# Optimization experiments

Measured on AMD Instinct MI355X. Metric: run time of the kernel, lower is better.

## Reference

```python
import jax, jax.numpy as jnp
import numpy as np

B, N, D = 4, 2048, 1024
H, DH = 16, 64
MAX_POS_EMB = 256
TOPK = 64


def setup_inputs() -> dict:
    key = jax.random.key(0)
    ks = jax.random.split(key, 8)
    s = 0.02
    inner = H * DH
    return {
        "x": jax.random.normal(ks[0], (B, N, D), jnp.float32),
        "gating_mask": jax.random.uniform(ks[1], (B, 1, N, 1), jnp.float32),
        "Wq": jax.random.normal(ks[2], (D, inner), jnp.float32) * s,
        "bq": jnp.zeros((inner,), jnp.float32),
        "Wkv": jax.random.normal(ks[3], (D, 2 * inner), jnp.float32) * s,
        "bkv": jnp.zeros((2 * inner,), jnp.float32),
        "Wo": jax.random.normal(ks[4], (inner, D), jnp.float32) * s,
        "bo": jnp.zeros((D,), jnp.float32),
        "rel_emb": jax.random.normal(ks[5], (MAX_POS_EMB, DH), jnp.float32) * s,
        "mask": jnp.ones((B, N), bool),
        "sparse_topk": TOPK,
    }


def reference(x, gating_mask, Wq, bq, Wkv, bkv, Wo, bo, rel_emb, mask, sparse_topk):
    b, n, d = x.shape
    h, dh = H, DH
    scale = dh ** -0.5
    mask_val = -jnp.finfo(x.dtype).max

    # projections -> [b, h, n, dh]
    q = (x @ Wq + bq).reshape(b, n, h, dh).transpose(0, 2, 1, 3)
    kv = x @ Wkv + bkv
    k = kv[..., : h * dh].reshape(b, n, h, dh).transpose(0, 2, 1, 3)
    v = kv[..., h * dh:].reshape(b, n, h, dh).transpose(0, 2, 1, 3)

    dots = jnp.einsum("bhid,bhjd->bhij", q, k) * scale  # [b,h,n,n]

    # relative positional bias: q . E[clip(i-j+M, 0, M-1)]
    seq = jnp.arange(n)
    dist = jnp.clip(seq[:, None] - seq[None, :] + MAX_POS_EMB, 0, MAX_POS_EMB - 1)
    qE = jnp.einsum("bhid,rd->bhir", q, rel_emb) * scale  # [b,h,n,R]
    pos_attn = jnp.take_along_axis(qE, dist[None, None, :, :], axis=-1)  # [b,h,n,n]
    dots = dots + pos_attn

    # padding mask: mask_i * mask_j
    full_mask = mask[:, None, :, None] & mask[:, None, None, :]
    dots = jnp.where(full_mask, dots, mask_val)

    # topk sparsification: keep only scores >= k-th largest per row
    top = jax.lax.top_k(dots, sparse_topk)[0]  # [b,h,n,topk]
    vk = top[..., -1:]
    dots = jnp.where(dots < vk, mask_val, dots)

    attn = jax.nn.softmax(dots, axis=-1)
    attn = attn * gating_mask

    out = jnp.einsum("bhij,bhjd->bhid", attn, v)
    out = out.transpose(0, 2, 1, 3).reshape(b, n, h * dh)
    return out @ Wo + bo
```

## Files before the change

kernel.cpp:

```cpp
#include <hip/hip_runtime.h>
#include <stdint.h>


typedef __attribute__((ext_vector_type(8))) short short8;
typedef __attribute__((ext_vector_type(4))) float floatx4;

#define Bn   4
#define Nn   2048
#define Hn   16
#define BHn  (Bn*Hn)
#define DELTA 0.00125f

__device__ __forceinline__ float bf2f(unsigned short u) {
  union { unsigned int i; float f; } v; v.i = ((unsigned int)u) << 16; return v.f;
}
__device__ __forceinline__ unsigned short f2bf(float f) {
  union { float f; unsigned int i; } v; v.f = f;
  unsigned int r = v.i + 0x7fffu + ((v.i >> 16) & 1u);
  return (unsigned short)(r >> 16);
}
__device__ __forceinline__ floatx4 mfma16(short8 a, short8 b, floatx4 c) {
  return __builtin_amdgcn_mfma_f32_16x16x32_bf16(a, b, c, 0, 0, 0);
}
__device__ __forceinline__ void split2(float x, unsigned short& h, unsigned short& m) {
  h = f2bf(x);
  m = f2bf(x - bf2f(h));
}
__device__ __forceinline__ void split3(float x, unsigned short& h, unsigned short& m, unsigned short& l) {
  h = f2bf(x);
  float r = x - bf2f(h);
  m = f2bf(r);
  l = f2bf(r - bf2f(m));
}

__global__ __launch_bounds__(256)
void transpose_split3(const float* __restrict__ W,
                      unsigned short* __restrict__ T0,
                      unsigned short* __restrict__ T1,
                      unsigned short* __restrict__ T2,
                      int K, int Ncols)
{
  __shared__ float tile[32][33];
  int k0 = blockIdx.y * 32, n0 = blockIdx.x * 32;
  int tx = threadIdx.x & 31, ty = threadIdx.x >> 5;
  for (int s = 0; s < 32; s += 8)
    tile[ty + s][tx] = W[(size_t)(k0 + ty + s) * Ncols + n0 + tx];
  __syncthreads();
  for (int s = 0; s < 32; s += 8) {
    float x = tile[tx][ty + s];
    unsigned short h, m, l;
    split3(x, h, m, l);
    size_t o = (size_t)(n0 + ty + s) * K + k0 + tx;
    T0[o] = h; T1[o] = m; T2[o] = l;
  }
}

__global__ __launch_bounds__(256)
void transpose_split2(const float* __restrict__ W,
                      unsigned short* __restrict__ T0,
                      unsigned short* __restrict__ T1,
                      int K, int Ncols)
{
  __shared__ float tile[32][33];
  int k0 = blockIdx.y * 32, n0 = blockIdx.x * 32;
  int tx = threadIdx.x & 31, ty = threadIdx.x >> 5;
  for (int s = 0; s < 32; s += 8)
    tile[ty + s][tx] = W[(size_t)(k0 + ty + s) * Ncols + n0 + tx];
  __syncthreads();
  for (int s = 0; s < 32; s += 8) {
    float x = tile[tx][ty + s];
    unsigned short h, m;
    split2(x, h, m);
    size_t o = (size_t)(n0 + ty + s) * K + k0 + tx;
    T0[o] = h; T1[o] = m;
  }
}

__global__ __launch_bounds__(256)
void convert_bf16(const float* __restrict__ in, unsigned short* __restrict__ outp, int n) {
  int i = blockIdx.x * 256 + threadIdx.x;
  if (i < n) outp[i] = f2bf(in[i]);
}

__global__ __launch_bounds__(256)
void gemm_qkv(const float* __restrict__ A,
              const unsigned short* __restrict__ B0,
              const unsigned short* __restrict__ B1,
              const unsigned short* __restrict__ B2,
              const float* __restrict__ bias,
              float* __restrict__ O32,
              unsigned short* __restrict__ Oh,
              unsigned short* __restrict__ Om,
              _Float16* __restrict__ Vh,
              int K, float scale)
{
  __shared__ unsigned short lA[3][128 * 40];
  __shared__ unsigned short lB[3][128 * 40];
  const int tid = threadIdx.x;
  const int lane = tid & 63;
  const int m0 = blockIdx.y * 128, n0 = blockIdx.x * 128;
  const bool vblk = (n0 >= 1024);
  const int wid = tid >> 6, wm = wid >> 1, wn = wid & 1;
  const int fr = lane & 15, fq = lane >> 4;
  floatx4 acc[4][4] = {};

  for (int k0 = 0; k0 < K; k0 += 32) {
    __syncthreads();
    #pragma unroll
    for (int p = 0; p < 2; p++) {
      int c = tid + p * 256;
      int row = c >> 2, kc = (c & 3) * 8;
      size_t go = (size_t)(m0 + row) * K + k0 + kc;
      float4 v0 = *(const float4*)&A[go];
      float4 v1 = *(const float4*)&A[go + 4];
      union { unsigned short u[8]; uint4 q; } hh, mm, ll;
      float xs[8] = {v0.x, v0.y, v0.z, v0.w, v1.x, v1.y, v1.z, v1.w};
      #pragma unroll
      for (int e = 0; e < 8; e++) split3(xs[e], hh.u[e], mm.u[e], ll.u[e]);
      *(uint4*)&lA[0][row * 40 + kc] = hh.q;
      *(uint4*)&lA[1][row * 40 + kc] = mm.q;
      size_t bo = (size_t)(n0 + row) * K + k0 + kc;
      *(uint4*)&lB[0][row * 40 + kc] = *(const uint4*)&B0[bo];
      *(uint4*)&lB[1][row * 40 + kc] = *(const uint4*)&B1[bo];
      if (!vblk) {
        *(uint4*)&lA[2][row * 40 + kc] = ll.q;
        *(uint4*)&lB[2][row * 40 + kc] = *(const uint4*)&B2[bo];
      }
    }
    __syncthreads();
    short8 af0[4], af1[4], af2[4], bf0[4], bf1[4], bf2v[4];
    #pragma unroll
    for (int t = 0; t < 4; t++) {
      int ao = (wm * 64 + t * 16 + fr) * 40 + 8 * fq;
      int bo2 = (wn * 64 + t * 16 + fr) * 40 + 8 * fq;
      af0[t] = *(const short8*)&lA[0][ao];
      af1[t] = *(const short8*)&lA[1][ao];
      bf0[t] = *(const short8*)&lB[0][bo2];
      bf1[t] = *(const short8*)&lB[1][bo2];
      if (!vblk) {
        af2[t] = *(const short8*)&lA[2][ao];
        bf2v[t] = *(const short8*)&lB[2][bo2];
      }
    }
    #pragma unroll
    for (int mi = 0; mi < 4; mi++)
      #pragma unroll
      for (int ni = 0; ni < 4; ni++) {
        acc[mi][ni] = mfma16(af0[mi], bf0[ni], acc[mi][ni]);
        acc[mi][ni] = mfma16(af0[mi], bf1[ni], acc[mi][ni]);
        acc[mi][ni] = mfma16(af1[mi], bf0[ni], acc[mi][ni]);
        if (!vblk) {
          acc[mi][ni] = mfma16(af1[mi], bf1[ni], acc[mi][ni]);
          acc[mi][ni] = mfma16(af0[mi], bf2v[ni], acc[mi][ni]);
          acc[mi][ni] = mfma16(af2[mi], bf0[ni], acc[mi][ni]);
        }
      }
  }
  #pragma unroll
  for (int mi = 0; mi < 4; mi++)
    #pragma unroll
    for (int ni = 0; ni < 4; ni++) {
      int nl = n0 + wn * 64 + ni * 16 + fr;
      float bv = bias[nl];
      #pragma unroll
      for (int rg = 0; rg < 4; rg++) {
        int ml = m0 + wm * 64 + mi * 16 + fq * 4 + rg;
        float val = (acc[mi][ni][rg] + bv) * scale;
        int bb = ml >> 11, ii = ml & 2047;
        int hh2 = (nl & 1023) >> 6, dd = nl & 63;
        size_t idx = (((size_t)bb * Hn + hh2) * Nn + ii) * 64 + dd;
        if (!vblk) {
          O32[idx] = val;
          unsigned short h, m;
          split2(val, h, m);
          Oh[idx] = h; Om[idx] = m;
        } else {
          Vh[idx] = (_Float16)val;
        }
      }
    }
}

__global__ __launch_bounds__(256)
void gemm_out(const float* __restrict__ A,
              const unsigned short* __restrict__ B0,
              const unsigned short* __restrict__ B1,
              const float* __restrict__ bias,
              float* __restrict__ O32,
              int Ncols, int K)
{
  __shared__ unsigned short lA[2][128 * 40];
  __shared__ unsigned short lB[2][128 * 40];
  const int tid = threadIdx.x;
  const int lane = tid & 63;
  const int m0 = blockIdx.y * 128, n0 = blockIdx.x * 128;
  const int wid = tid >> 6, wm = wid >> 1, wn = wid & 1;
  const int fr = lane & 15, fq = lane >> 4;
  floatx4 acc[4][4] = {};

  for (int k0 = 0; k0 < K; k0 += 32) {
    __syncthreads();
    #pragma unroll
    for (int p = 0; p < 2; p++) {
      int c = tid + p * 256;
      int row = c >> 2, kc = (c & 3) * 8;
      size_t go = (size_t)(m0 + row) * K + k0 + kc;
      float4 v0 = *(const float4*)&A[go];
      float4 v1 = *(const float4*)&A[go + 4];
      union { unsigned short u[8]; uint4 q; } hh, mm;
      float xs[8] = {v0.x, v0.y, v0.z, v0.w, v1.x, v1.y, v1.z, v1.w};
      #pragma unroll
      for (int e = 0; e < 8; e++) split2(xs[e], hh.u[e], mm.u[e]);
      *(uint4*)&lA[0][row * 40 + kc] = hh.q;
      *(uint4*)&lA[1][row * 40 + kc] = mm.q;
      size_t bo = (size_t)(n0 + row) * K + k0 + kc;
      *(uint4*)&lB[0][row * 40 + kc] = *(const uint4*)&B0[bo];
      *(uint4*)&lB[1][row * 40 + kc] = *(const uint4*)&B1[bo];
    }
    __syncthreads();
    short8 af[2][4], bfr[2][4];
    #pragma unroll
    for (int s = 0; s < 2; s++)
      #pragma unroll
      for (int t = 0; t < 4; t++) {
        af[s][t]  = *(const short8*)&lA[s][(wm * 64 + t * 16 + fr) * 40 + 8 * fq];
        bfr[s][t] = *(const short8*)&lB[s][(wn * 64 + t * 16 + fr) * 40 + 8 * fq];
      }
    #pragma unroll
    for (int mi = 0; mi < 4; mi++)
      #pragma unroll
      for (int ni = 0; ni < 4; ni++) {
        acc[mi][ni] = mfma16(af[0][mi], bfr[0][ni], acc[mi][ni]);
        acc[mi][ni] = mfma16(af[0][mi], bfr[1][ni], acc[mi][ni]);
        acc[mi][ni] = mfma16(af[1][mi], bfr[0][ni], acc[mi][ni]);
      }
  }
  #pragma unroll
  for (int mi = 0; mi < 4; mi++)
    #pragma unroll
    for (int ni = 0; ni < 4; ni++) {
      int nl = n0 + wn * 64 + ni * 16 + fr;
      float bv = bias[nl];
      #pragma unroll
      for (int rg = 0; rg < 4; rg++) {
        int ml = m0 + wm * 64 + mi * 16 + fq * 4 + rg;
        O32[(size_t)ml * Ncols + nl] = acc[mi][ni][rg] + bv;
      }
    }
}

__global__ __launch_bounds__(1024, 8)
void attn_k(const unsigned short* __restrict__ qh,
            const unsigned short* __restrict__ qm,
            const unsigned short* __restrict__ kh,
            const unsigned short* __restrict__ km,
            const _Float16* __restrict__ vh,
            const float* __restrict__ q32,
            const float* __restrict__ k32,
            const unsigned short* __restrict__ relbf,
            const float* __restrict__ rel32,
            const float* __restrict__ gating,
            const int* __restrict__ topkp,
            float* __restrict__ inner)
{
  extern __shared__ char smem[];
  _Float16* S = (_Float16*)smem;
  unsigned short* KtH = (unsigned short*)(smem + 65536);
  unsigned short* KtM = KtH + 4096;
  _Float16* qE = (_Float16*)KtH;

  const int ib = blockIdx.x, bh = blockIdx.y;
  const int i0 = ib * 16;
  const int b = bh >> 4, h = bh & 15;
  const int tid = threadIdx.x;
  const int lane = tid & 63, w = tid >> 6;
  const int fr = lane & 15, fq = lane >> 4;
  const int topk = topkp[0];

  const size_t qoff = ((size_t)bh * Nn + i0) * 64;
  const size_t qf = qoff + (size_t)fr * 64 + 8 * fq;
  const short8 aqh0 = *(const short8*)&qh[qf];
  const short8 aqh1 = *(const short8*)&qh[qf + 32];
  const short8 aqm0 = *(const short8*)&qm[qf];
  const short8 aqm1 = *(const short8*)&qm[qf + 32];

  for (int jt = 0; jt < 32; jt++) {
    __syncthreads();
    {
      int sel = tid >> 9;
      int row = (tid >> 3) & 63, ch = tid & 7;
      int dst = row * 64 + ((ch ^ (row & 7)) * 8);
      size_t g = ((size_t)bh * Nn + jt * 64 + row) * 64 + ch * 8;
      unsigned short* T = sel ? KtM : KtH;
      const unsigned short* src = sel ? km : kh;
      *(uint4*)&T[dst] = *(const uint4*)&src[g];
    }
    __syncthreads();
    if (w < 8 && ((jt & 1) == (w >> 2))) {
      int wc = w & 3;
      int row16 = wc * 16 + fr, r7 = fr & 7;
      int b0 = row16 * 64 + ((fq ^ r7) * 8);
      int b1 = row16 * 64 + (((fq + 4) ^ r7) * 8);
      short8 kh0 = *(const short8*)&KtH[b0];
      short8 kh1 = *(const short8*)&KtH[b1];
      short8 km0 = *(const short8*)&KtM[b0];
      short8 km1 = *(const short8*)&KtM[b1];
      floatx4 c = {};
      c = mfma16(aqh0, kh0, c); c = mfma16(aqh1, kh1, c);
      c = mfma16(aqh0, km0, c); c = mfma16(aqh1, km1, c);
      c = mfma16(aqm0, kh0, c); c = mfma16(aqm1, kh1, c);
      int colsw = jt * 64 + ((wc ^ fq) * 16) + fr;
      #pragma unroll
      for (int rg = 0; rg < 4; rg++)
        S[(fq * 4 + rg) * 2048 + colsw] = (_Float16)c[rg];
    }
  }
  __syncthreads();

  {
    size_t rf = (size_t)(w * 16 + fr) * 64 + 8 * fq;
    short8 rb0 = *(const short8*)&relbf[rf];
    short8 rb1 = *(const short8*)&relbf[rf + 32];
    floatx4 c = {};
    c = mfma16(aqh0, rb0, c); c = mfma16(aqh1, rb1, c);
    c = mfma16(aqm0, rb0, c); c = mfma16(aqm1, rb1, c);
    int colsw = ((w ^ fq) * 16) + fr;
    #pragma unroll
    for (int rg = 0; rg < 4; rg++)
      qE[(fq * 4 + rg) * 256 + colsw] = (_Float16)c[rg];
  }
  __syncthreads();

  const int r = w;
  const int i = i0 + r;
  const int X = (r >> 2) << 4;
  _Float16* S0 = S + r * 2048;
  const _Float16* qE0 = qE + r * 256;
  const float cA = (float)qE0[255 ^ X], cC = (float)qE0[X];
  const int swl = (2 * lane) ^ X;

  float key[32];
  float mx = -3.0e38f, sm = 0.f, sq = 0.f;
  #pragma unroll
  for (int e = 0; e < 16; e++) {
    const int jb = 128 * e;
    union { unsigned int u; _Float16 hx[2]; } u0;
    u0.u = *(const unsigned int*)&S0[jb + swl];
    const int j0 = jb + 2 * lane;
    float e0, e1;
    if (jb + 127 <= i) { e0 = cA; e1 = cA; }
    else if (jb >= i + 256) { e0 = cC; e1 = cC; }
    else {
      int c0 = i - j0 + 256; c0 = c0 < 0 ? 0 : (c0 > 255 ? 255 : c0);
      int c1 = i - j0 + 255; c1 = c1 < 0 ? 0 : (c1 > 255 ? 255 : c1);
      e0 = (float)qE0[c0 ^ X]; e1 = (float)qE0[c1 ^ X];
    }
    float a0 = (float)u0.hx[0] + e0, a1 = (float)u0.hx[1] + e1;
    key[2 * e] = a0; key[2 * e + 1] = a1;
    mx = fmaxf(mx, fmaxf(a0, a1));
    sm += a0 + a1;
    sq = fmaf(a0, a0, fmaf(a1, a1, sq));
  }
  #pragma unroll
  for (int d = 1; d < 64; d <<= 1) {
    mx = fmaxf(mx, __shfl_xor(mx, d));
    sm += __shfl_xor(sm, d);
    sq += __shfl_xor(sq, d);
  }
  const float mu = sm * (1.f / 2048.f);
  const float sg = sqrtf(fmaxf(sq * (1.f / 2048.f) - mu * mu, 0.f)) + 1e-9f;

  auto cntGE = [&](float u) -> int {
    int c = 0;
    #pragma unroll
    for (int t = 0; t < 32; t++) c += (key[t] >= u) ? 1 : 0;
    #pragma unroll
    for (int d = 1; d < 64; d <<= 1) c += __shfl_xor(c, d);
    return c;
  };

  float lo = mu + 1.6f * sg;
  float hi = mx + fabsf(mx) * 1e-6f + 1e-20f;
  if (cntGE(lo) < topk) {
    lo = mu;
    if (cntGE(lo) < topk) lo = mu - 20.f * sg;
  }
  #pragma unroll 1
  for (int it = 0; it < 10; it++) {
    float mid = 0.5f * (lo + hi);
    if (cntGE(mid) >= topk) lo = mid; else hi = mid;
  }
  const float C = hi + 2.f * DELTA, L = lo - 2.f * DELTA;

  char* sb = (char*)S0;
  float* Pl = (float*)sb;          int* Jl = (int*)(sb + 512);
  float* Sx = (float*)(sb + 1024); int* Jc = (int*)(sb + 1280);
  asm volatile("" ::: "memory");
  const unsigned long long lmlt = (1ull << lane) - 1ull;

  int base = 0, mc = 0;
  #pragma unroll
  for (int t = 0; t < 32; t++) {
    const int j = 2 * lane + 128 * (t >> 1) + (t & 1);
    bool dk = key[t] >= C;
    bool cd = (key[t] >= L) && !dk;
    unsigned long long mk = __ballot(dk);
    if (dk) { int pos = base + __popcll(mk & lmlt); Pl[pos] = key[t]; Jl[pos] = j; }
    base += __popcll(mk);
    mk = __ballot(cd);
    if (cd) { int pos = mc + __popcll(mk & lmlt); if (pos < 64) Jc[pos] = j; }
    mc += __popcll(mk);
  }
  if (mc > 64) mc = 64;
  asm volatile("" ::: "memory");

  const double qv = (double)q32[((size_t)bh * Nn + i) * 64 + lane];
  #pragma unroll 1
  for (int c2 = 0; c2 < mc; c2++) {
    int j = Jc[c2];
    int ridx = i - j + 256; ridx = ridx < 0 ? 0 : (ridx > 255 ? 255 : ridx);
    double t = qv * ((double)k32[((size_t)bh * Nn + j) * 64 + lane] +
                     (double)rel32[ridx * 64 + lane]);
    #pragma unroll
    for (int d = 1; d < 64; d <<= 1) t += __shfl_xor(t, d);
    if (lane == 0) Sx[c2] = (float)t;
  }
  asm volatile("" ::: "memory");

  const int need = topk - base;
  float myx = (lane < mc) ? Sx[lane] : -3.0e38f;
  int rank = 0;
  #pragma unroll 1
  for (int c2 = 0; c2 < mc; c2++) {
    float o = Sx[c2];
    rank += (o > myx || (o == myx && c2 < lane)) ? 1 : 0;
  }
  unsigned long long bm = __ballot((lane < mc) && (rank == need - 1));
  float vk = bm ? __shfl(myx, (int)__ffsll(bm) - 1) : 3.0e38f;
  bool ck = (lane < mc) && ((rank < need) || (myx == vk));
  unsigned long long km2 = __ballot(ck);
  if (ck) { int pos = base + __popcll(km2 & lmlt); Pl[pos] = myx; Jl[pos] = Jc[lane]; }
  const int nk = base + __popcll(km2);
  asm volatile("" ::: "memory");

  float ps = 0.f;
  #pragma unroll 1
  for (int t = lane; t < nk; t += 64) { float p = __expf(Pl[t] - mx); Pl[t] = p; ps += p; }
  #pragma unroll
  for (int d = 1; d < 64; d <<= 1) ps += __shfl_xor(ps, d);
  const float coef = gating[(size_t)b * Nn + i] / ps;
  asm volatile("" ::: "memory");

  const _Float16* vbp = vh + (size_t)bh * Nn * 64 + lane;
  float a0 = 0.f, a1 = 0.f, a2 = 0.f, a3 = 0.f;
  int t4 = nk & ~3;
  #pragma unroll 1
  for (int t = 0; t < t4; t += 4) {
    float p0 = Pl[t], p1 = Pl[t + 1], p2 = Pl[t + 2], p3 = Pl[t + 3];
    int j0 = Jl[t], j1 = Jl[t + 1], j2 = Jl[t + 2], j3 = Jl[t + 3];
    a0 += p0 * (float)vbp[(size_t)j0 * 64];
    a1 += p1 * (float)vbp[(size_t)j1 * 64];
    a2 += p2 * (float)vbp[(size_t)j2 * 64];
    a3 += p3 * (float)vbp[(size_t)j3 * 64];
  }
  #pragma unroll 1
  for (int t = t4; t < nk; t++) a0 += Pl[t] * (float)vbp[(size_t)Jl[t] * 64];
  inner[((size_t)b * Nn + i) * 1024 + h * 64 + lane] = (a0 + a1 + a2 + a3) * coef;
}

extern "C" void kernel_launch(void* const* d_in, const int* in_sizes, int n_in,
                              void* d_out, int out_size, void* d_ws, size_t ws_size,
                              hipStream_t stream) {
  const float* x      = (const float*)d_in[0];
  const float* gating = (const float*)d_in[1];
  const float* Wq     = (const float*)d_in[2];
  const float* bq     = (const float*)d_in[3];
  const float* Wkv    = (const float*)d_in[4];
  const float* bkv    = (const float*)d_in[5];
  const float* Wo     = (const float*)d_in[6];
  const float* bo     = (const float*)d_in[7];
  const float* rel    = (const float*)d_in[8];
  const int*   topk   = (const int*)d_in[10];
  float* out = (float*)d_out;

  char* ws = (char*)d_ws;
  size_t off = 0;
  auto alloc = [&](size_t bytes) -> void* {
    void* p = ws + off; off += (bytes + 255) & ~(size_t)255; return p;
  };
  unsigned short* Wqt0 = (unsigned short*)alloc(1024ull * 1024 * 2);
  unsigned short* Wqt1 = (unsigned short*)alloc(1024ull * 1024 * 2);
  unsigned short* Wqt2 = (unsigned short*)alloc(1024ull * 1024 * 2);
  unsigned short* Wkt0 = (unsigned short*)alloc(2048ull * 1024 * 2);
  unsigned short* Wkt1 = (unsigned short*)alloc(2048ull * 1024 * 2);
  unsigned short* Wkt2 = (unsigned short*)alloc(2048ull * 1024 * 2);
  unsigned short* Wot0 = (unsigned short*)alloc(1024ull * 1024 * 2);
  unsigned short* Wot1 = (unsigned short*)alloc(1024ull * 1024 * 2);
  unsigned short* relbf = (unsigned short*)alloc(256ull * 64 * 2);
  float* q32 = (float*)alloc((size_t)BHn * Nn * 64 * 4);
  float* k32 = (float*)alloc((size_t)BHn * Nn * 64 * 4);
  unsigned short* qhb = (unsigned short*)alloc((size_t)BHn * Nn * 64 * 2);
  unsigned short* qmb = (unsigned short*)alloc((size_t)BHn * Nn * 64 * 2);
  unsigned short* khb = (unsigned short*)alloc((size_t)BHn * Nn * 64 * 2);
  unsigned short* kmb = (unsigned short*)alloc((size_t)BHn * Nn * 64 * 2);
  _Float16* vhb = (_Float16*)alloc((size_t)BHn * Nn * 64 * 2);
  float* inner = (float*)alloc((size_t)Bn * Nn * 1024 * 4);
  if (off > ws_size) return;

  size_t shmem = 65536 + 16384;
  (void)hipFuncSetAttribute((const void*)attn_k,
                            hipFuncAttributeMaxDynamicSharedMemorySize, (int)shmem);

  transpose_split3<<<dim3(32, 32), 256, 0, stream>>>(Wq, Wqt0, Wqt1, Wqt2, 1024, 1024);
  transpose_split3<<<dim3(64, 32), 256, 0, stream>>>(Wkv, Wkt0, Wkt1, Wkt2, 1024, 2048);
  transpose_split2<<<dim3(32, 32), 256, 0, stream>>>(Wo, Wot0, Wot1, 1024, 1024);
  convert_bf16<<<dim3(64), 256, 0, stream>>>(rel, relbf, 256 * 64);

  gemm_qkv<<<dim3(8, 64), 256, 0, stream>>>(x, Wqt0, Wqt1, Wqt2, bq,
      q32, qhb, qmb, vhb, 1024, 0.125f);
  gemm_qkv<<<dim3(16, 64), 256, 0, stream>>>(x, Wkt0, Wkt1, Wkt2, bkv,
      k32, khb, kmb, vhb, 1024, 1.0f);

  attn_k<<<dim3(128, 64), 1024, shmem, stream>>>(qhb, qmb, khb, kmb, vhb,
      q32, k32, relbf, rel, gating, topk, inner);

  gemm_out<<<dim3(8, 64), 256, 0, stream>>>(inner, Wot0, Wot1, bo,
      out, 1024, 1024);
}
```

Baseline: 1.174 ms.

## Load K directly per wave and bisect top-k threshold on packed fp16 keys

The QK score phase no longer stages K tiles through shared memory with two block barriers per tile. Instead each of the 16 waves loads its own K fragments from global memory and computes two 64-column tiles, which also shrinks the LDS allocation. The per-row top-k threshold search now packs fp16 scores into order-preserving 16-bit integer codes, two per register. It runs a fixed 13-step integer bisection instead of the mean/stddev-seeded float bisection. The candidate margin DELTA is doubled to cover the coarser fp16 grid, which may send more candidates to the exact fp64 re-score path, and K tiles are now read redundantly from global memory rather than shared.

```diff
diff --git a/kernel.cpp b/kernel.cpp
--- a/kernel.cpp
+++ b/kernel.cpp
@@ -4,12 +4,13 @@
 
 typedef __attribute__((ext_vector_type(8))) short short8;
 typedef __attribute__((ext_vector_type(4))) float floatx4;
+typedef _Float16 f16x2 __attribute__((ext_vector_type(2)));
 
 #define Bn   4
 #define Nn   2048
 #define Hn   16
 #define BHn  (Bn*Hn)
-#define DELTA 0.00125f
+#define DELTA 0.0025f
 
 __device__ __forceinline__ float bf2f(unsigned short u) {
   union { unsigned int i; float f; } v; v.i = ((unsigned int)u) << 16; return v.f;
@@ -31,6 +32,16 @@
   float r = x - bf2f(h);
   m = f2bf(r);
   l = f2bf(r - bf2f(m));
+}
+__device__ __forceinline__ unsigned int mapf(float f) {
+  union { _Float16 h; unsigned short s; } u; u.h = (_Float16)f;
+  unsigned int b = (unsigned int)u.s;
+  return (b & 0x8000u) ? (b ^ 0xFFFFu) : (b | 0x8000u);
+}
+__device__ __forceinline__ float unmapf(unsigned int c) {
+  unsigned int b = (c & 0x8000u) ? (c ^ 0x8000u) : (c ^ 0xFFFFu);
+  union { _Float16 h; unsigned short s; } u; u.s = (unsigned short)b;
+  return (float)u.h;
 }
 
 __global__ __launch_bounds__(256)
@@ -265,9 +276,7 @@
 {
   extern __shared__ char smem[];
   _Float16* S = (_Float16*)smem;
-  unsigned short* KtH = (unsigned short*)(smem + 65536);
-  unsigned short* KtM = KtH + 4096;
-  _Float16* qE = (_Float16*)KtH;
+  _Float16* qE = (_Float16*)(smem + 65536);
 
   const int ib = blockIdx.x, bh = blockIdx.y;
   const int i0 = ib * 16;
@@ -284,38 +293,27 @@
   const short8 aqm0 = *(const short8*)&qm[qf];
   const short8 aqm1 = *(const short8*)&qm[qf + 32];
 
-  for (int jt = 0; jt < 32; jt++) {
-    __syncthreads();
-    {
-      int sel = tid >> 9;
-      int row = (tid >> 3) & 63, ch = tid & 7;
-      int dst = row * 64 + ((ch ^ (row & 7)) * 8);
-      size_t g = ((size_t)bh * Nn + jt * 64 + row) * 64 + ch * 8;
-      unsigned short* T = sel ? KtM : KtH;
-      const unsigned short* src = sel ? km : kh;
-      *(uint4*)&T[dst] = *(const uint4*)&src[g];
-    }
-    __syncthreads();
-    if (w < 8 && ((jt & 1) == (w >> 2))) {
-      int wc = w & 3;
-      int row16 = wc * 16 + fr, r7 = fr & 7;
-      int b0 = row16 * 64 + ((fq ^ r7) * 8);
-      int b1 = row16 * 64 + (((fq + 4) ^ r7) * 8);
-      short8 kh0 = *(const short8*)&KtH[b0];
-      short8 kh1 = *(const short8*)&KtH[b1];
-      short8 km0 = *(const short8*)&KtM[b0];
-      short8 km1 = *(const short8*)&KtM[b1];
+  const size_t kbase = (size_t)bh * Nn * 64;
+  #pragma unroll 1
+  for (int t2 = 0; t2 < 2; t2++) {
+    const int jt = w * 2 + t2;
+    #pragma unroll 1
+    for (int wc = 0; wc < 4; wc++) {
+      const size_t kf = kbase + (size_t)(jt * 64 + wc * 16 + fr) * 64 + 8 * fq;
+      short8 bh0 = *(const short8*)&kh[kf];
+      short8 bh1 = *(const short8*)&kh[kf + 32];
+      short8 bm0 = *(const short8*)&km[kf];
+      short8 bm1 = *(const short8*)&km[kf + 32];
       floatx4 c = {};
-      c = mfma16(aqh0, kh0, c); c = mfma16(aqh1, kh1, c);
-      c = mfma16(aqh0, km0, c); c = mfma16(aqh1, km1, c);
-      c = mfma16(aqm0, kh0, c); c = mfma16(aqm1, kh1, c);
+      c = mfma16(aqh0, bh0, c); c = mfma16(aqh1, bh1, c);
+      c = mfma16(aqh0, bm0, c); c = mfma16(aqh1, bm1, c);
+      c = mfma16(aqm0, bh0, c); c = mfma16(aqm1, bh1, c);
       int colsw = jt * 64 + ((wc ^ fq) * 16) + fr;
       #pragma unroll
       for (int rg = 0; rg < 4; rg++)
         S[(fq * 4 + rg) * 2048 + colsw] = (_Float16)c[rg];
     }
   }
-  __syncthreads();
 
   {
     size_t rf = (size_t)(w * 16 + fr) * 64 + 8 * fq;
@@ -336,76 +334,84 @@
   const int X = (r >> 2) << 4;
   _Float16* S0 = S + r * 2048;
   const _Float16* qE0 = qE + r * 256;
-  const float cA = (float)qE0[255 ^ X], cC = (float)qE0[X];
+  union pun { unsigned int u; f16x2 h; };
+  pun cAp, cCp;
+  cAp.h[0] = qE0[255 ^ X]; cAp.h[1] = cAp.h[0];
+  cCp.h[0] = qE0[X];       cCp.h[1] = cCp.h[0];
   const int swl = (2 * lane) ^ X;
 
-  float key[32];
-  float mx = -3.0e38f, sm = 0.f, sq = 0.f;
+  unsigned int kk[16];
+  unsigned int mh = 0, ml = 0;
   #pragma unroll
   for (int e = 0; e < 16; e++) {
     const int jb = 128 * e;
-    union { unsigned int u; _Float16 hx[2]; } u0;
-    u0.u = *(const unsigned int*)&S0[jb + swl];
-    const int j0 = jb + 2 * lane;
-    float e0, e1;
-    if (jb + 127 <= i) { e0 = cA; e1 = cA; }
-    else if (jb >= i + 256) { e0 = cC; e1 = cC; }
+    pun sv, ev;
+    sv.u = *(const unsigned int*)&S0[jb + swl];
+    if (jb + 127 <= i) ev = cAp;
+    else if (jb >= i + 256) ev = cCp;
     else {
+      const int j0 = jb + 2 * lane;
       int c0 = i - j0 + 256; c0 = c0 < 0 ? 0 : (c0 > 255 ? 255 : c0);
       int c1 = i - j0 + 255; c1 = c1 < 0 ? 0 : (c1 > 255 ? 255 : c1);
-      e0 = (float)qE0[c0 ^ X]; e1 = (float)qE0[c1 ^ X];
-    }
-    float a0 = (float)u0.hx[0] + e0, a1 = (float)u0.hx[1] + e1;
-    key[2 * e] = a0; key[2 * e + 1] = a1;
-    mx = fmaxf(mx, fmaxf(a0, a1));
-    sm += a0 + a1;
-    sq = fmaf(a0, a0, fmaf(a1, a1, sq));
-  }
+      ev.h[0] = qE0[c0 ^ X]; ev.h[1] = qE0[c1 ^ X];
+    }
+    pun rv; rv.h = sv.h + ev.h;
+    unsigned int u = rv.u;
+    unsigned int sgn = (u >> 15) & 0x00010001u;
+    unsigned int code = u ^ (sgn * 0x7FFFu + 0x80008000u);
+    kk[e] = code;
+    unsigned int chi = code & 0xFFFF0000u, clo = code << 16;
+    mh = mh > chi ? mh : chi;
+    ml = ml > clo ? ml : clo;
+  }
+  unsigned int umax = (mh > ml ? mh : ml) >> 16;
+  unsigned int mxu = umax, mnu = umax;
   #pragma unroll
   for (int d = 1; d < 64; d <<= 1) {
-    mx = fmaxf(mx, __shfl_xor(mx, d));
-    sm += __shfl_xor(sm, d);
-    sq += __shfl_xor(sq, d);
-  }
-  const float mu = sm * (1.f / 2048.f);
-  const float sg = sqrtf(fmaxf(sq * (1.f / 2048.f) - mu * mu, 0.f)) + 1e-9f;
-
-  auto cntGE = [&](float u) -> int {
-    int c = 0;
-    #pragma unroll
-    for (int t = 0; t < 32; t++) c += (key[t] >= u) ? 1 : 0;
-    #pragma unroll
-    for (int d = 1; d < 64; d <<= 1) c += __shfl_xor(c, d);
-    return c;
-  };
-
-  float lo = mu + 1.6f * sg;
-  float hi = mx + fabsf(mx) * 1e-6f + 1e-20f;
-  if (cntGE(lo) < topk) {
-    lo = mu;
-    if (cntGE(lo) < topk) lo = mu - 20.f * sg;
-  }
-  #pragma unroll 1
-  for (int it = 0; it < 10; it++) {
-    float mid = 0.5f * (lo + hi);
-    if (cntGE(mid) >= topk) lo = mid; else hi = mid;
-  }
-  const float C = hi + 2.f * DELTA, L = lo - 2.f * DELTA;
+    unsigned int o1 = (unsigned int)__shfl_xor((int)mxu, d);
+    unsigned int o2 = (unsigned int)__shfl_xor((int)mnu, d);
+    mxu = o1 > mxu ? o1 : mxu;
+    mnu = o2 < mnu ? o2 : mnu;
+  }
+  const float mxv = unmapf(mxu);
+
+  unsigned int lo = mnu, hi = mxu + 1;
+  #pragma unroll 1
+  for (int it = 0; it < 13; it++) {
+    unsigned int mid = (lo + hi) >> 1;
+    int cnt = 0;
+    #pragma unroll
+    for (int e = 0; e < 16; e++) {
+      cnt += ((kk[e] & 0xffffu) >= mid) ? 1 : 0;
+      cnt += ((kk[e] >> 16) >= mid) ? 1 : 0;
+    }
+    #pragma unroll
+    for (int d = 1; d < 64; d <<= 1) cnt += __shfl_xor(cnt, d);
+    if (cnt >= topk) lo = mid; else hi = mid;
+  }
+  const float Cv = unmapf(hi) + 2.0f * DELTA;
+  const float Lv = unmapf(lo) - 2.0f * DELTA;
+  const unsigned int Cu = mapf(Cv) + 1;
+  int Lsi = (int)mapf(Lv) - 1;
+  const unsigned int Lu = Lsi < 0 ? 0u : (unsigned int)Lsi;
 
   char* sb = (char*)S0;
-  float* Pl = (float*)sb;          int* Jl = (int*)(sb + 512);
-  float* Sx = (float*)(sb + 1024); int* Jc = (int*)(sb + 1280);
+  unsigned int* Pk = (unsigned int*)sb;
+  int*   Jc = (int*)(sb + 512);
+  float* Sx = (float*)(sb + 768);
+  float* P2 = (float*)(sb + 1024);
   asm volatile("" ::: "memory");
   const unsigned long long lmlt = (1ull << lane) - 1ull;
 
   int base = 0, mc = 0;
   #pragma unroll
   for (int t = 0; t < 32; t++) {
+    unsigned int code = (t & 1) ? (kk[t >> 1] >> 16) : (kk[t >> 1] & 0xffffu);
     const int j = 2 * lane + 128 * (t >> 1) + (t & 1);
-    bool dk = key[t] >= C;
-    bool cd = (key[t] >= L) && !dk;
+    bool dk = code >= Cu;
+    bool cd = (code >= Lu) && !dk;
     unsigned long long mk = __ballot(dk);
-    if (dk) { int pos = base + __popcll(mk & lmlt); Pl[pos] = key[t]; Jl[pos] = j; }
+    if (dk) { int pos = base + __popcll(mk & lmlt); Pk[pos] = (unsigned int)j | (code << 16); }
     base += __popcll(mk);
     mk = __ballot(cd);
     if (cd) { int pos = mc + __popcll(mk & lmlt); if (pos < 64) Jc[pos] = j; }
@@ -419,11 +425,11 @@
   for (int c2 = 0; c2 < mc; c2++) {
     int j = Jc[c2];
     int ridx = i - j + 256; ridx = ridx < 0 ? 0 : (ridx > 255 ? 255 : ridx);
-    double t = qv * ((double)k32[((size_t)bh * Nn + j) * 64 + lane] +
-                     (double)rel32[ridx * 64 + lane]);
-    #pragma unroll
-    for (int d = 1; d < 64; d <<= 1) t += __shfl_xor(t, d);
-    if (lane == 0) Sx[c2] = (float)t;
+    double t2 = qv * ((double)k32[((size_t)bh * Nn + j) * 64 + lane] +
+                      (double)rel32[ridx * 64 + lane]);
+    #pragma unroll
+    for (int d = 1; d < 64; d <<= 1) t2 += __shfl_xor(t2, d);
+    if (lane == 0) Sx[c2] = (float)t2;
   }
   asm volatile("" ::: "memory");
 
@@ -439,13 +445,21 @@
   float vk = bm ? __shfl(myx, (int)__ffsll(bm) - 1) : 3.0e38f;
   bool ck = (lane < mc) && ((rank < need) || (myx == vk));
   unsigned long long km2 = __ballot(ck);
-  if (ck) { int pos = base + __popcll(km2 & lmlt); Pl[pos] = myx; Jl[pos] = Jc[lane]; }
+  float pb = 0.f;
+  if (ck) {
+    int pos = base + __popcll(km2 & lmlt);
+    Pk[pos] = (unsigned int)Jc[lane];
+    pb = __expf(myx - mxv);
+    P2[pos] = pb;
+  }
   const int nk = base + __popcll(km2);
-  asm volatile("" ::: "memory");
-
-  float ps = 0.f;
-  #pragma unroll 1
-  for (int t = lane; t < nk; t += 64) { float p = __expf(Pl[t] - mx); Pl[t] = p; ps += p; }
+  float ps = pb;
+  #pragma unroll 1
+  for (int t = lane; t < base; t += 64) {
+    float val = unmapf(Pk[t] >> 16);
+    float p = __expf(val - mxv);
+    P2[t] = p; ps += p;
+  }
   #pragma unroll
   for (int d = 1; d < 64; d <<= 1) ps += __shfl_xor(ps, d);
   const float coef = gating[(size_t)b * Nn + i] / ps;
@@ -456,15 +470,17 @@
   int t4 = nk & ~3;
   #pragma unroll 1
   for (int t = 0; t < t4; t += 4) {
-    float p0 = Pl[t], p1 = Pl[t + 1], p2 = Pl[t + 2], p3 = Pl[t + 3];
-    int j0 = Jl[t], j1 = Jl[t + 1], j2 = Jl[t + 2], j3 = Jl[t + 3];
+    int j0 = (int)(Pk[t] & 0xffffu), j1 = (int)(Pk[t + 1] & 0xffffu);
+    int j2 = (int)(Pk[t + 2] & 0xffffu), j3 = (int)(Pk[t + 3] & 0xffffu);
+    float p0 = P2[t], p1 = P2[t + 1], p2 = P2[t + 2], p3 = P2[t + 3];
     a0 += p0 * (float)vbp[(size_t)j0 * 64];
     a1 += p1 * (float)vbp[(size_t)j1 * 64];
     a2 += p2 * (float)vbp[(size_t)j2 * 64];
     a3 += p3 * (float)vbp[(size_t)j3 * 64];
   }
   #pragma unroll 1
-  for (int t = t4; t < nk; t++) a0 += Pl[t] * (float)vbp[(size_t)Jl[t] * 64];
+  for (int t = t4; t < nk; t++)
+    a0 += P2[t] * (float)vbp[(size_t)(Pk[t] & 0xffffu) * 64];
   inner[((size_t)b * Nn + i) * 1024 + h * 64 + lane] = (a0 + a1 + a2 + a3) * coef;
 }
 
@@ -507,7 +523,7 @@
   float* inner = (float*)alloc((size_t)Bn * Nn * 1024 * 4);
   if (off > ws_size) return;
 
-  size_t shmem = 65536 + 16384;
+  size_t shmem = 65536 + 8192;
   (void)hipFuncSetAttribute((const void*)attn_k,
                             hipFuncAttributeMaxDynamicSharedMemorySize, (int)shmem);
 
```

After: 1.345 ms. 14.6% more time.

## Load K fragments directly from global and simplify top-k threshold search

Applied to the files above, without the earlier changes.

The QK score stage no longer stages K tiles through shared memory behind two block barriers per tile. Each wave now computes its own pair of 64-column tiles, reading bf16 hi/mid K fragments straight from global memory. The top-k threshold search drops the mean/variance-based bracket and instead bisects for 12 steps from the row min to the row max, counting with ballot+popcount. Shared memory shrinks and the launch bound changes to 4, trading barrier stalls for uncached-by-LDS global loads and possibly more bisection iterations.

```diff
diff --git a/kernel.cpp b/kernel.cpp
--- a/kernel.cpp
+++ b/kernel.cpp
@@ -249,7 +249,7 @@
     }
 }
 
-__global__ __launch_bounds__(1024, 8)
+__global__ __launch_bounds__(1024, 4)
 void attn_k(const unsigned short* __restrict__ qh,
             const unsigned short* __restrict__ qm,
             const unsigned short* __restrict__ kh,
@@ -265,9 +265,7 @@
 {
   extern __shared__ char smem[];
   _Float16* S = (_Float16*)smem;
-  unsigned short* KtH = (unsigned short*)(smem + 65536);
-  unsigned short* KtM = KtH + 4096;
-  _Float16* qE = (_Float16*)KtH;
+  _Float16* qE = (_Float16*)(smem + 65536);
 
   const int ib = blockIdx.x, bh = blockIdx.y;
   const int i0 = ib * 16;
@@ -284,38 +282,34 @@
   const short8 aqm0 = *(const short8*)&qm[qf];
   const short8 aqm1 = *(const short8*)&qm[qf + 32];
 
-  for (int jt = 0; jt < 32; jt++) {
-    __syncthreads();
-    {
-      int sel = tid >> 9;
-      int row = (tid >> 3) & 63, ch = tid & 7;
-      int dst = row * 64 + ((ch ^ (row & 7)) * 8);
-      size_t g = ((size_t)bh * Nn + jt * 64 + row) * 64 + ch * 8;
-      unsigned short* T = sel ? KtM : KtH;
-      const unsigned short* src = sel ? km : kh;
-      *(uint4*)&T[dst] = *(const uint4*)&src[g];
-    }
-    __syncthreads();
-    if (w < 8 && ((jt & 1) == (w >> 2))) {
-      int wc = w & 3;
-      int row16 = wc * 16 + fr, r7 = fr & 7;
-      int b0 = row16 * 64 + ((fq ^ r7) * 8);
-      int b1 = row16 * 64 + (((fq + 4) ^ r7) * 8);
-      short8 kh0 = *(const short8*)&KtH[b0];
-      short8 kh1 = *(const short8*)&KtH[b1];
-      short8 km0 = *(const short8*)&KtM[b0];
-      short8 km1 = *(const short8*)&KtM[b1];
+  const size_t kbase = (size_t)bh * Nn * 64;
+  #pragma unroll 1
+  for (int t2 = 0; t2 < 2; t2++) {
+    const int jt = w * 2 + t2;
+    #pragma unroll 1
+    for (int wc = 0; wc < 4; wc++) {
+      const size_t kf = kbase + (size_t)(jt * 64 + wc * 16 + fr) * 64 + 8 * fq;
       floatx4 c = {};
-      c = mfma16(aqh0, kh0, c); c = mfma16(aqh1, kh1, c);
-      c = mfma16(aqh0, km0, c); c = mfma16(aqh1, km1, c);
-      c = mfma16(aqm0, kh0, c); c = mfma16(aqm1, kh1, c);
+      {
+        short8 b0 = *(const short8*)&kh[kf];
+        short8 b1 = *(const short8*)&kh[kf + 32];
+        c = mfma16(aqh0, b0, c);
+        c = mfma16(aqm0, b0, c);
+        c = mfma16(aqh1, b1, c);
+        c = mfma16(aqm1, b1, c);
+      }
+      {
+        short8 b0 = *(const short8*)&km[kf];
+        short8 b1 = *(const short8*)&km[kf + 32];
+        c = mfma16(aqh0, b0, c);
+        c = mfma16(aqh1, b1, c);
+      }
       int colsw = jt * 64 + ((wc ^ fq) * 16) + fr;
       #pragma unroll
       for (int rg = 0; rg < 4; rg++)
         S[(fq * 4 + rg) * 2048 + colsw] = (_Float16)c[rg];
     }
   }
-  __syncthreads();
 
   {
     size_t rf = (size_t)(w * 16 + fr) * 64 + 8 * fq;
@@ -340,7 +334,7 @@
   const int swl = (2 * lane) ^ X;
 
   float key[32];
-  float mx = -3.0e38f, sm = 0.f, sq = 0.f;
+  float lmax = -3.0e38f;
   #pragma unroll
   for (int e = 0; e < 16; e++) {
     const int jb = 128 * e;
@@ -357,38 +351,25 @@
     }
     float a0 = (float)u0.hx[0] + e0, a1 = (float)u0.hx[1] + e1;
     key[2 * e] = a0; key[2 * e + 1] = a1;
-    mx = fmaxf(mx, fmaxf(a0, a1));
-    sm += a0 + a1;
-    sq = fmaf(a0, a0, fmaf(a1, a1, sq));
-  }
+    lmax = fmaxf(lmax, fmaxf(a0, a1));
+  }
+  float mx = lmax, mn = lmax;
   #pragma unroll
   for (int d = 1; d < 64; d <<= 1) {
     mx = fmaxf(mx, __shfl_xor(mx, d));
-    sm += __shfl_xor(sm, d);
-    sq += __shfl_xor(sq, d);
-  }
-  const float mu = sm * (1.f / 2048.f);
-  const float sg = sqrtf(fmaxf(sq * (1.f / 2048.f) - mu * mu, 0.f)) + 1e-9f;
-
-  auto cntGE = [&](float u) -> int {
-    int c = 0;
-    #pragma unroll
-    for (int t = 0; t < 32; t++) c += (key[t] >= u) ? 1 : 0;
-    #pragma unroll
-    for (int d = 1; d < 64; d <<= 1) c += __shfl_xor(c, d);
-    return c;
-  };
-
-  float lo = mu + 1.6f * sg;
+    mn = fminf(mn, __shfl_xor(mn, d));
+  }
+
+  float lo = mn;
   float hi = mx + fabsf(mx) * 1e-6f + 1e-20f;
-  if (cntGE(lo) < topk) {
-    lo = mu;
-    if (cntGE(lo) < topk) lo = mu - 20.f * sg;
-  }
-  #pragma unroll 1
-  for (int it = 0; it < 10; it++) {
+  #pragma unroll 1
+  for (int it = 0; it < 12; it++) {
     float mid = 0.5f * (lo + hi);
-    if (cntGE(mid) >= topk) lo = mid; else hi = mid;
+    int cnt = 0;
+    #pragma unroll
+    for (int t = 0; t < 32; t++)
+      cnt += (int)__popcll(__ballot(key[t] >= mid));
+    if (cnt >= topk) lo = mid; else hi = mid;
   }
   const float C = hi + 2.f * DELTA, L = lo - 2.f * DELTA;
 
@@ -419,11 +400,11 @@
   for (int c2 = 0; c2 < mc; c2++) {
     int j = Jc[c2];
     int ridx = i - j + 256; ridx = ridx < 0 ? 0 : (ridx > 255 ? 255 : ridx);
-    double t = qv * ((double)k32[((size_t)bh * Nn + j) * 64 + lane] +
-                     (double)rel32[ridx * 64 + lane]);
-    #pragma unroll
-    for (int d = 1; d < 64; d <<= 1) t += __shfl_xor(t, d);
-    if (lane == 0) Sx[c2] = (float)t;
+    double t2 = qv * ((double)k32[((size_t)bh * Nn + j) * 64 + lane] +
+                      (double)rel32[ridx * 64 + lane]);
+    #pragma unroll
+    for (int d = 1; d < 64; d <<= 1) t2 += __shfl_xor(t2, d);
+    if (lane == 0) Sx[c2] = (float)t2;
   }
   asm volatile("" ::: "memory");
 
@@ -507,7 +488,7 @@
   float* inner = (float*)alloc((size_t)Bn * Nn * 1024 * 4);
   if (off > ws_size) return;
 
-  size_t shmem = 65536 + 16384;
+  size_t shmem = 65536 + 8192;
   (void)hipFuncSetAttribute((const void*)attn_k,
                             hipFuncAttributeMaxDynamicSharedMemorySize, (int)shmem);
 
```

Result: slower. 1.561 ms (+33.0%).
